# Optimization experiments

Measured on AMD Instinct MI355X. Metric: run time of the kernel, lower is better.

Reference implementation:

```python
import jax, jax.numpy as jnp
import numpy as np

IN_FEATURES = 4096
OUT_FEATURES = 4096
B, S = 4, 2048


def setup_inputs() -> dict:
    key = jax.random.key(0)
    k_x, k_w, k_ws, k_ss, k_b = jax.random.split(key, 5)
    x = jax.random.normal(k_x, (B, S, IN_FEATURES), dtype=jnp.float32)
    weight_quantized = jax.random.randint(k_w, (OUT_FEATURES, IN_FEATURES), -128, 128, dtype=jnp.int32).astype(jnp.int8)
    # realistic per-output-channel weight scales (small positive)
    weight_scale = jax.random.uniform(k_ws, (OUT_FEATURES,), dtype=jnp.float32, minval=1e-3, maxval=2e-2)
    # smoothing scales near 1 (clamped to [0.01, 100] in from_float)
    smooth_scale = jax.random.uniform(k_ss, (IN_FEATURES,), dtype=jnp.float32, minval=0.5, maxval=2.0)
    bias = 0.01 * jax.random.normal(k_b, (OUT_FEATURES,), dtype=jnp.float32)
    return {"x": x, "weight_quantized": weight_quantized, "weight_scale": weight_scale,
            "smooth_scale": smooth_scale, "bias": bias}


def reference(x, weight_quantized, weight_scale, smooth_scale, bias):
    # per-tensor dynamic activation quantization after smooth-scale divide
    x_smooth = x / smooth_scale                                   # [B,S,in]
    act_scale = jnp.max(jnp.abs(x_smooth)) / 127.0                # scalar
    x_quant = jnp.clip(jnp.round(x_smooth / (act_scale + 1e-5)), -128, 127).astype(jnp.int8)
    # int8 GEMM emulated in fp32 (matches torch reference: F.linear on float casts)
    out = jnp.einsum('bsi,oi->bso', x_quant.astype(jnp.float32),
                     weight_quantized.astype(jnp.float32))        # [B,S,out]
    out = out * act_scale * weight_scale                          # fused dequant
    return out + bias
```

## Files before the change

kernel.cpp:

```cpp
#include <hip/hip_runtime.h>
#include <stdint.h>

#define M_TOT 8192
#define N_TOT 4096
#define K_TOT 4096

typedef int v4i __attribute__((ext_vector_type(4)));

#define BM 256
#define BN 256
#define SUB 64
#define NS (K_TOT / SUB)
#define A_SUB (BM * SUB)
#define B_SUB (BN * SUB)
#define BUF_BYTES (A_SUB + B_SUB)

__global__ void pack_w(const int4* __restrict__ w32, int* __restrict__ w8, int n4,
                       const float* __restrict__ smooth, float* __restrict__ rcp) {
  if (blockIdx.x == 0) {
    for (int i = threadIdx.x; i < K_TOT; i += blockDim.x) rcp[i] = 1.0f / smooth[i];
  }
  int stride = gridDim.x * blockDim.x;
  for (int i = blockIdx.x * blockDim.x + threadIdx.x; i < n4; i += stride) {
    int4 v = w32[i];
    w8[i] = (v.x & 0xff) | ((v.y & 0xff) << 8) | ((v.z & 0xff) << 16) | (v.w << 24);
  }
}

__global__ void reduce_maxabs(const float4* __restrict__ x,
                              const float4* __restrict__ rcp4,
                              unsigned int* __restrict__ maxbits, int n4) {
  float m = 0.0f;
  int stride = gridDim.x * blockDim.x;
  for (int i = blockIdx.x * blockDim.x + threadIdx.x; i < n4; i += stride) {
    float4 v = x[i];
    float4 r = rcp4[i & (K_TOT / 4 - 1)];
    m = fmaxf(m, fabsf(v.x * r.x));
    m = fmaxf(m, fabsf(v.y * r.y));
    m = fmaxf(m, fabsf(v.z * r.z));
    m = fmaxf(m, fabsf(v.w * r.w));
  }
#pragma unroll
  for (int off = 32; off; off >>= 1) m = fmaxf(m, __shfl_xor(m, off));
  __shared__ float sm[4];
  if ((threadIdx.x & 63) == 0) sm[threadIdx.x >> 6] = m;
  __syncthreads();
  if (threadIdx.x == 0) {
    float mm = fmaxf(fmaxf(sm[0], sm[1]), fmaxf(sm[2], sm[3]));
    atomicMax(maxbits, __float_as_uint(mm));
  }
}

__global__ void quantize_x(const float4* __restrict__ x,
                           const float4* __restrict__ rcp4,
                           const unsigned int* __restrict__ maxbits,
                           int* __restrict__ xq, int n4) {
  const float d = __uint_as_float(*maxbits) / 127.0f + 1e-5f;
  const float inv = 1.0f / d;
  int stride = gridDim.x * blockDim.x;
  for (int i = blockIdx.x * blockDim.x + threadIdx.x; i < n4; i += stride) {
    float4 v = x[i];
    float4 r = rcp4[i & (K_TOT / 4 - 1)];
    int q0 = (int)fminf(fmaxf(rintf(v.x * r.x * inv), -128.0f), 127.0f);
    int q1 = (int)fminf(fmaxf(rintf(v.y * r.y * inv), -128.0f), 127.0f);
    int q2 = (int)fminf(fmaxf(rintf(v.z * r.z * inv), -128.0f), 127.0f);
    int q3 = (int)fminf(fmaxf(rintf(v.w * r.w * inv), -128.0f), 127.0f);
    xq[i] = (q0 & 0xff) | ((q1 & 0xff) << 8) | ((q2 & 0xff) << 16) | (q3 << 24);
  }
}

__global__ __launch_bounds__(512, 2) void gemm_i8(
    const int8_t* __restrict__ Aq,
    const int8_t* __restrict__ Wt,
    const unsigned int* __restrict__ maxbits,
    const float* __restrict__ wscale,
    const float* __restrict__ bias,
    float* __restrict__ out) {
  __shared__ int8_t lds[4 * BUF_BYTES];

  const int tid = threadIdx.x;
  const int lane = tid & 63;
  const int wid = tid >> 6;
  const int l16 = lane & 15;
  const int lhi = lane >> 4;

  const int flat = blockIdx.y * gridDim.x + blockIdx.x;
  const int swz = (flat & 7) * 64 + (flat >> 3);
  const int m0 = (swz / (N_TOT / BN)) * BM;
  const int n0 = (swz % (N_TOT / BN)) * BN;

  const int wave_m = wid >> 2;
  const int wave_n = wid & 3;

  const int row_l = lane >> 2;
  const int gcol = ((lane & 3) ^ lhi) << 4;
  const int8_t* Abase = Aq + (size_t)m0 * K_TOT;
  const int8_t* Bbase = Wt + (size_t)n0 * K_TOT;
  int goff[2];
#pragma unroll
  for (int c = 0; c < 2; ++c) {
    int grow = (wid * 2 + c) * 16 + row_l;
    goff[c] = grow * K_TOT + gcol;
  }

  auto stage = [&](int dstbuf, int koff) {
#pragma unroll
    for (int c = 0; c < 2; ++c) {
      __builtin_amdgcn_global_load_lds(
          (const __attribute__((address_space(1))) void*)(Abase + goff[c] + koff),
          (__attribute__((address_space(3))) void*)(lds + dstbuf * BUF_BYTES + (wid * 2 + c) * 1024),
          16, 0, 0);
      __builtin_amdgcn_global_load_lds(
          (const __attribute__((address_space(1))) void*)(Bbase + goff[c] + koff),
          (__attribute__((address_space(3))) void*)(lds + dstbuf * BUF_BYTES + A_SUB + (wid * 2 + c) * 1024),
          16, 0, 0);
    }
  };

  const int slot = (lhi ^ ((l16 >> 2) & 3)) << 4;
  const int aOff = (wave_m * 128 + l16) * SUB + slot;
  const int bOff = (wave_n * 64 + l16) * SUB + slot;

  stage(0, 0);
  stage(1, SUB);
  stage(2, 2 * SUB);
  asm volatile("s_waitcnt vmcnt(8)" ::: "memory");
  __builtin_amdgcn_s_barrier();
  __builtin_amdgcn_sched_barrier(0);

  v4i acc[8][4] = {};

#pragma unroll 4
  for (int s = 0; s < NS; ++s) {
    const int buf = s & 3;
    const int8_t* Ab = lds + buf * BUF_BYTES;
    const int8_t* Bb = Ab + A_SUB;

    const int ts = (s + 3 < NS) ? (s + 3) : (NS - 1);
    stage((s + 3) & 3, ts * SUB);

    v4i a[8], b[4];
#pragma unroll
    for (int i = 0; i < 8; ++i) a[i] = *(const v4i*)(Ab + aOff + i * 1024);
#pragma unroll
    for (int j = 0; j < 4; ++j) b[j] = *(const v4i*)(Bb + bOff + j * 1024);

    __builtin_amdgcn_s_setprio(1);
#pragma unroll
    for (int i = 0; i < 8; ++i)
#pragma unroll
      for (int j = 0; j < 4; ++j)
        acc[i][j] = __builtin_amdgcn_mfma_i32_16x16x64_i8(a[i], b[j], acc[i][j], 0, 0, 0);
    __builtin_amdgcn_s_setprio(0);
    __builtin_amdgcn_sched_barrier(0);

    asm volatile("s_waitcnt lgkmcnt(0)" ::: "memory");
    asm volatile("s_waitcnt vmcnt(8)" ::: "memory");
    __builtin_amdgcn_sched_barrier(0);
    __builtin_amdgcn_s_barrier();
    __builtin_amdgcn_sched_barrier(0);
  }

  const float ascale = __uint_as_float(*maxbits) / 127.0f;
#pragma unroll
  for (int i = 0; i < 8; ++i) {
    const int orow = m0 + wave_m * 128 + i * 16 + lhi * 4;
#pragma unroll
    for (int j = 0; j < 4; ++j) {
      const int ocol = n0 + wave_n * 64 + j * 16 + l16;
      const float wsc = wscale[ocol] * ascale;
      const float bb = bias[ocol];
#pragma unroll
      for (int r = 0; r < 4; ++r) {
        out[(size_t)(orow + r) * N_TOT + ocol] = (float)acc[i][j][r] * wsc + bb;
      }
    }
  }
}

extern "C" void kernel_launch(void* const* d_in, const int* in_sizes, int n_in,
                              void* d_out, int out_size, void* d_ws, size_t ws_size,
                              hipStream_t stream) {
  const float* x = (const float*)d_in[0];
  const int* w32 = (const int*)d_in[1];
  const float* wscale = (const float*)d_in[2];
  const float* smooth = (const float*)d_in[3];
  const float* bias = (const float*)d_in[4];
  float* out = (float*)d_out;

  unsigned int* maxbits = (unsigned int*)d_ws;
  float* rcp = (float*)((char*)d_ws + 1024);
  int8_t* xq = (int8_t*)d_ws + (1 << 20);
  int8_t* wq8 = xq + (size_t)M_TOT * K_TOT;

  hipMemsetAsync(d_ws, 0, 4, stream);

  const int nw4 = N_TOT * K_TOT / 4;
  pack_w<<<2048, 256, 0, stream>>>((const int4*)w32, (int*)wq8, nw4, smooth, rcp);

  const int n4 = M_TOT * K_TOT / 4;
  reduce_maxabs<<<2048, 256, 0, stream>>>((const float4*)x, (const float4*)rcp,
                                          maxbits, n4);
  quantize_x<<<2048, 256, 0, stream>>>((const float4*)x, (const float4*)rcp,
                                       maxbits, (int*)xq, n4);

  dim3 grid(N_TOT / BN, M_TOT / BM);
  gemm_i8<<<grid, 512, 0, stream>>>(xq, wq8, maxbits, wscale, bias, out);
}
```

Before: 243.8 us.

## Fuse weight packing with max-abs reduction and retune LDS swizzle pattern

Weight int32-to-int8 packing and the activation max-abs reduction are merged into one kernel, removing a launch and letting both bandwidth-bound loops share one pass. The fused reduction divides by smooth_scale directly instead of reading the reciprocals, since those are now produced by the same kernel without a grid-wide sync. The GEMM's LDS XOR swizzle is changed on both the global-to-LDS write and the fragment read side, to reduce LDS bank conflicts. Dividing per element costs more ALU than multiplying, but the loop is memory-bound.

```diff
diff --git a/kernel.cpp b/kernel.cpp
--- a/kernel.cpp
+++ b/kernel.cpp
@@ -15,30 +15,28 @@
 #define B_SUB (BN * SUB)
 #define BUF_BYTES (A_SUB + B_SUB)
 
-__global__ void pack_w(const int4* __restrict__ w32, int* __restrict__ w8, int n4,
-                       const float* __restrict__ smooth, float* __restrict__ rcp) {
+__global__ void prep_reduce(const int4* __restrict__ w32, int* __restrict__ w8,
+                            int nw4, const float* __restrict__ smooth,
+                            float* __restrict__ rcp, const float4* __restrict__ x,
+                            unsigned int* __restrict__ maxbits, int nx4) {
   if (blockIdx.x == 0) {
     for (int i = threadIdx.x; i < K_TOT; i += blockDim.x) rcp[i] = 1.0f / smooth[i];
   }
-  int stride = gridDim.x * blockDim.x;
-  for (int i = blockIdx.x * blockDim.x + threadIdx.x; i < n4; i += stride) {
+  const int stride = gridDim.x * blockDim.x;
+  const int g0 = blockIdx.x * blockDim.x + threadIdx.x;
+  for (int i = g0; i < nw4; i += stride) {
     int4 v = w32[i];
     w8[i] = (v.x & 0xff) | ((v.y & 0xff) << 8) | ((v.z & 0xff) << 16) | (v.w << 24);
   }
-}
-
-__global__ void reduce_maxabs(const float4* __restrict__ x,
-                              const float4* __restrict__ rcp4,
-                              unsigned int* __restrict__ maxbits, int n4) {
+  const float4* smooth4 = (const float4*)smooth;
   float m = 0.0f;
-  int stride = gridDim.x * blockDim.x;
-  for (int i = blockIdx.x * blockDim.x + threadIdx.x; i < n4; i += stride) {
+  for (int i = g0; i < nx4; i += stride) {
     float4 v = x[i];
-    float4 r = rcp4[i & (K_TOT / 4 - 1)];
-    m = fmaxf(m, fabsf(v.x * r.x));
-    m = fmaxf(m, fabsf(v.y * r.y));
-    m = fmaxf(m, fabsf(v.z * r.z));
-    m = fmaxf(m, fabsf(v.w * r.w));
+    float4 s = smooth4[i & (K_TOT / 4 - 1)];
+    m = fmaxf(m, fabsf(v.x / s.x));
+    m = fmaxf(m, fabsf(v.y / s.y));
+    m = fmaxf(m, fabsf(v.z / s.z));
+    m = fmaxf(m, fabsf(v.w / s.w));
   }
 #pragma unroll
   for (int off = 32; off; off >>= 1) m = fmaxf(m, __shfl_xor(m, off));
@@ -93,7 +91,7 @@
   const int wave_n = wid & 3;
 
   const int row_l = lane >> 2;
-  const int gcol = ((lane & 3) ^ lhi) << 4;
+  const int gcol = ((lane & 3) ^ ((lane >> 3) & 3)) << 4;
   const int8_t* Abase = Aq + (size_t)m0 * K_TOT;
   const int8_t* Bbase = Wt + (size_t)n0 * K_TOT;
   int goff[2];
@@ -117,7 +115,7 @@
     }
   };
 
-  const int slot = (lhi ^ ((l16 >> 2) & 3)) << 4;
+  const int slot = (lhi ^ ((l16 >> 1) & 3)) << 4;
   const int aOff = (wave_m * 128 + l16) * SUB + slot;
   const int bOff = (wave_n * 64 + l16) * SUB + slot;
 
@@ -196,11 +194,10 @@
   hipMemsetAsync(d_ws, 0, 4, stream);
 
   const int nw4 = N_TOT * K_TOT / 4;
-  pack_w<<<2048, 256, 0, stream>>>((const int4*)w32, (int*)wq8, nw4, smooth, rcp);
-
   const int n4 = M_TOT * K_TOT / 4;
-  reduce_maxabs<<<2048, 256, 0, stream>>>((const float4*)x, (const float4*)rcp,
-                                          maxbits, n4);
+  prep_reduce<<<2048, 256, 0, stream>>>((const int4*)w32, (int*)wq8, nw4,
+                                        smooth, rcp, (const float4*)x,
+                                        maxbits, n4);
   quantize_x<<<2048, 256, 0, stream>>>((const float4*)x, (const float4*)rcp,
                                        maxbits, (int*)xq, n4);
 
```

Measured after the change: 224.9 us. -7.7%, faster.
